# Optimization experiments

Measured on AMD Instinct MI355X. Metric: run time of the kernel, lower is better.

The kernel has to match this reference:

```python
import jax, jax.numpy as jnp
import numpy as np

N_EXPERTS = 8
D_MODEL = 512
HIDDEN = 1408
TOTAL_TOKENS = 32768  # 4096 tokens per expert, equal contiguous segments


def setup_inputs() -> dict:
    key = jax.random.key(0)
    k1, k2, k3 = jax.random.split(key, 3)
    sorted_x = jax.random.normal(k1, (TOTAL_TOKENS, D_MODEL), dtype=jnp.float32)
    # weights init: normal(std=0.02) as in the torch module
    w12 = 0.02 * jax.random.normal(k2, (N_EXPERTS, 2 * HIDDEN, D_MODEL), dtype=jnp.float32)
    w3 = 0.02 * jax.random.normal(k3, (N_EXPERTS, D_MODEL, HIDDEN), dtype=jnp.float32)
    tpe = TOTAL_TOKENS // N_EXPERTS
    expert_starts = jnp.arange(N_EXPERTS, dtype=jnp.int32) * tpe
    expert_ends = expert_starts + tpe
    return {"sorted_x": sorted_x, "w12": w12, "w3": w3,
            "expert_starts": expert_starts, "expert_ends": expert_ends}


def reference(sorted_x, w12, w3, expert_starts, expert_ends):
    """Grouped SwiGLU expert MLP over tokens pre-sorted by expert.

    setup_inputs() produces equal-sized contiguous expert segments, so each
    expert processes tpe = T // E tokens (fixed-size grouped GEMM).
    """
    E, twoH, D = w12.shape
    T = sorted_x.shape[0]
    tpe = T // E  # tokens per expert segment

    # gather each expert's contiguous token block: (E, tpe, D)
    x_e = jax.vmap(lambda s: jax.lax.dynamic_slice(sorted_x, (s, 0), (tpe, D)))(expert_starts)

    # grouped GEMM 1 (fused gate+up): (E, tpe, 2H)
    h12 = jnp.einsum('etd,ehd->eth', x_e, w12).astype(jnp.float32)
    h1, h2 = jnp.split(h12, 2, axis=-1)
    h = jax.nn.silu(h1) * h2  # SwiGLU

    # grouped GEMM 2 (down-proj): (E, tpe, D)
    out = jnp.einsum('eth,edh->etd', h.astype(sorted_x.dtype), w3).astype(jnp.float32)
    # segments are contiguous and in expert order -> concat == reshape
    return out.reshape(T, D)
```

## Files before the change

kernel.cpp:

```cpp
#include <hip/hip_runtime.h>
#include <stdint.h>

#define TPE 4096
#define DM 512
#define HID 1408
#define NE 8

#define N4X   4194304
#define N4W12 2883584

typedef unsigned short u16;
typedef __attribute__((ext_vector_type(8))) __bf16 bf16x8;
typedef __attribute__((ext_vector_type(4))) float f32x4;

__device__ __forceinline__ u16 f2bf(float f) {
  union { float f; uint32_t u; } v; v.f = f;
  uint32_t u = v.u;
  u += 0x7fffu + ((u >> 16) & 1u);
  return (u16)(u >> 16);
}

__global__ void cvt_xw12(const float* __restrict__ x, const float* __restrict__ w12,
                         u16* __restrict__ xb, u16* __restrict__ w12b) {
  int i = blockIdx.x * blockDim.x + threadIdx.x;
  const float* src; u16* dst; int off;
  if (i < N4X) { src = x;   dst = xb;   off = i; }
  else         { src = w12; dst = w12b; off = i - N4X; }
  float4 v = reinterpret_cast<const float4*>(src)[off];
  union { u16 s[4]; uint2 u2; } o;
  o.s[0] = f2bf(v.x); o.s[1] = f2bf(v.y); o.s[2] = f2bf(v.z); o.s[3] = f2bf(v.w);
  reinterpret_cast<uint2*>(dst)[off] = o.u2;
}

template <int ROWS>
__device__ __forceinline__ void stage_tile64(u16* lds, const u16* g, int lda,
                                             int wave, int lane) {
  const int srow = lane >> 3;
  const int gchunk = (lane & 7) ^ srow;
#pragma unroll
  for (int r = 0; r < ROWS / 32; ++r) {
    const int row0 = (wave * (ROWS / 32) + r) * 8;
    const u16* gp = g + (size_t)(row0 + srow) * lda + gchunk * 8;
    u16* lp = lds + row0 * 64;
    __builtin_amdgcn_global_load_lds((const __attribute__((address_space(1))) void*)gp,
                                     (__attribute__((address_space(3))) void*)lp,
                                     16, 0, 0);
  }
}

__device__ __forceinline__ void stage256(u16* lds, const u16* g, int lda,
                                         int wave, int lane) {
  const int srow = lane >> 3;
  const int gchunk = (lane & 7) ^ srow;
#pragma unroll
  for (int r = 0; r < 4; ++r) {
    const int row0 = (r * 8 + wave) * 8;
    const u16* gp = g + (size_t)(row0 + srow) * lda + gchunk * 8;
    u16* lp = lds + row0 * 64;
    __builtin_amdgcn_global_load_lds((const __attribute__((address_space(1))) void*)gp,
                                     (__attribute__((address_space(3))) void*)lp,
                                     16, 0, 0);
  }
}

__device__ __forceinline__ void stageB256(u16* lds, const u16* Bg, const u16* Bu,
                                          int wave, int lane) {
  const int srow = lane >> 3;
  const int gchunk = (lane & 7) ^ srow;
#pragma unroll
  for (int r = 0; r < 4; ++r) {
    const int rowblk = r * 8 + wave;
    const int row0 = rowblk * 8;
    const u16* base = (rowblk < 16) ? (Bg + (size_t)row0 * DM)
                                    : (Bu + (size_t)(row0 - 128) * DM);
    const u16* gp = base + (size_t)srow * DM + gchunk * 8;
    u16* lp = lds + row0 * 64;
    __builtin_amdgcn_global_load_lds((const __attribute__((address_space(1))) void*)gp,
                                     (__attribute__((address_space(3))) void*)lp,
                                     16, 0, 0);
  }
}

__device__ __forceinline__ bf16x8 read_frag(const u16* lds, int row, int kchunk) {
  return *reinterpret_cast<const bf16x8*>(&lds[row * 64 + (((kchunk ^ (row & 7)) << 3))]);
}

__global__ __launch_bounds__(512, 2)
void gemm1_swiglu(const u16* __restrict__ xb, const u16* __restrict__ w12b,
                  u16* __restrict__ hb, const float* __restrict__ w3f,
                  u16* __restrict__ w3b) {
  __shared__ u16 sA[2][256 * 64];
  __shared__ u16 sB[2][256 * 64];
  const int e = blockIdx.x;
  const int y = blockIdx.y;
  const int tid = threadIdx.x;

  if (y >= 176) {
    const int c = e + 8 * (y - 176);
    const float4* src = reinterpret_cast<const float4*>(w3f) + (size_t)c * 4096;
    uint2* dst = reinterpret_cast<uint2*>(w3b) + (size_t)c * 4096;
#pragma unroll
    for (int it = 0; it < 8; ++it) {
      float4 v = src[it * 512 + tid];
      union { u16 s[4]; uint2 u2; } o;
      o.s[0] = f2bf(v.x); o.s[1] = f2bf(v.y); o.s[2] = f2bf(v.z); o.s[3] = f2bf(v.w);
      dst[it * 512 + tid] = o.u2;
    }
    return;
  }

  const int mt = y / 11, nt = y % 11;
  const int wave = tid >> 6, lane = tid & 63;
  const int wm = wave >> 2, wn = wave & 3;
  const int quad = lane >> 4, rr = lane & 15;

  const u16* A  = xb + (size_t)(e * TPE + mt * 256) * DM;
  const u16* Bg = w12b + (size_t)e * (2 * HID) * DM + (size_t)(nt * 128) * DM;
  const u16* Bu = Bg + (size_t)HID * DM;

  f32x4 zero = {0.f, 0.f, 0.f, 0.f};
  f32x4 accg[8][2], accu[8][2];
#pragma unroll
  for (int i = 0; i < 8; ++i)
#pragma unroll
    for (int j = 0; j < 2; ++j) { accg[i][j] = zero; accu[i][j] = zero; }

  stage256(sA[0], A, DM, wave, lane);
  stageB256(sB[0], Bg, Bu, wave, lane);
  __syncthreads();

#pragma unroll 2
  for (int t = 0; t < 8; ++t) {
    const int cur = t & 1, nxt = cur ^ 1;
    const u16* cA = sA[cur];
    const u16* cB = sB[cur];
    bf16x8 af[4][2], bg[2][2], bu[2][2];

    if (t < 7) stage256(sA[nxt], A + (t + 1) * 64, DM, wave, lane);
#pragma unroll
    for (int mi = 0; mi < 4; ++mi)
#pragma unroll
      for (int kk = 0; kk < 2; ++kk)
        af[mi][kk] = read_frag(cA, wm * 128 + mi * 16 + rr, kk * 4 + quad);
#pragma unroll
    for (int ni = 0; ni < 2; ++ni)
#pragma unroll
      for (int kk = 0; kk < 2; ++kk)
        bg[ni][kk] = read_frag(cB, wn * 32 + ni * 16 + rr, kk * 4 + quad);
    __builtin_amdgcn_s_barrier();
    __builtin_amdgcn_s_setprio(1);
#pragma unroll
    for (int mi = 0; mi < 4; ++mi)
#pragma unroll
      for (int ni = 0; ni < 2; ++ni)
#pragma unroll
        for (int kk = 0; kk < 2; ++kk)
          accg[mi][ni] = __builtin_amdgcn_mfma_f32_16x16x32_bf16(af[mi][kk], bg[ni][kk], accg[mi][ni], 0, 0, 0);
    __builtin_amdgcn_s_setprio(0);
    __builtin_amdgcn_s_barrier();

    if (t < 7) stageB256(sB[nxt], Bg + (t + 1) * 64, Bu + (t + 1) * 64, wave, lane);
#pragma unroll
    for (int ni = 0; ni < 2; ++ni)
#pragma unroll
      for (int kk = 0; kk < 2; ++kk)
        bu[ni][kk] = read_frag(cB, 128 + wn * 32 + ni * 16 + rr, kk * 4 + quad);
    __builtin_amdgcn_s_barrier();
    __builtin_amdgcn_s_setprio(1);
#pragma unroll
    for (int mi = 0; mi < 4; ++mi)
#pragma unroll
      for (int ni = 0; ni < 2; ++ni)
#pragma unroll
        for (int kk = 0; kk < 2; ++kk)
          accu[mi][ni] = __builtin_amdgcn_mfma_f32_16x16x32_bf16(af[mi][kk], bu[ni][kk], accu[mi][ni], 0, 0, 0);
    __builtin_amdgcn_s_setprio(0);
    __builtin_amdgcn_s_barrier();

#pragma unroll
    for (int mi = 0; mi < 4; ++mi)
#pragma unroll
      for (int kk = 0; kk < 2; ++kk)
        af[mi][kk] = read_frag(cA, wm * 128 + 64 + mi * 16 + rr, kk * 4 + quad);
    __builtin_amdgcn_s_barrier();
    __builtin_amdgcn_s_setprio(1);
#pragma unroll
    for (int mi = 0; mi < 4; ++mi)
#pragma unroll
      for (int ni = 0; ni < 2; ++ni)
#pragma unroll
        for (int kk = 0; kk < 2; ++kk)
          accg[4 + mi][ni] = __builtin_amdgcn_mfma_f32_16x16x32_bf16(af[mi][kk], bg[ni][kk], accg[4 + mi][ni], 0, 0, 0);
    __builtin_amdgcn_s_setprio(0);
    __builtin_amdgcn_s_barrier();

    __builtin_amdgcn_s_setprio(1);
#pragma unroll
    for (int mi = 0; mi < 4; ++mi)
#pragma unroll
      for (int ni = 0; ni < 2; ++ni)
#pragma unroll
        for (int kk = 0; kk < 2; ++kk)
          accu[4 + mi][ni] = __builtin_amdgcn_mfma_f32_16x16x32_bf16(af[mi][kk], bu[ni][kk], accu[4 + mi][ni], 0, 0, 0);
    __builtin_amdgcn_s_setprio(0);
    __syncthreads();
  }

  const size_t rowbase = (size_t)(e * TPE + mt * 256 + wm * 128);
  const int colbase = nt * 128 + wn * 32;
#pragma unroll
  for (int mi = 0; mi < 8; ++mi)
#pragma unroll
    for (int ni = 0; ni < 2; ++ni)
#pragma unroll
      for (int r2 = 0; r2 < 4; ++r2) {
        float g = accg[mi][ni][r2];
        float u = accu[mi][ni][r2];
        float s = (g / (1.f + __expf(-g))) * u;
        size_t row = rowbase + mi * 16 + quad * 4 + r2;
        int col = colbase + ni * 16 + rr;
        hb[row * HID + col] = f2bf(s);
      }
}

__global__ __launch_bounds__(256, 2)
void gemm2(const u16* __restrict__ hb, const u16* __restrict__ w3b,
           float* __restrict__ out) {
  __shared__ u16 sA[128 * 64];
  __shared__ u16 sB[256 * 64];
  const int e = blockIdx.x;
  const int mt = blockIdx.y >> 1, nt = blockIdx.y & 1;
  const int tid = threadIdx.x, wave = tid >> 6, lane = tid & 63;
  const int wm = wave >> 1, wn = wave & 1;
  const int quad = lane >> 4, rr = lane & 15;

  const u16* A = hb + (size_t)(e * TPE + mt * 128) * HID;
  const u16* B = w3b + (size_t)e * DM * HID + (size_t)(nt * 256) * HID;

  f32x4 zero = {0.f, 0.f, 0.f, 0.f};
  f32x4 acc[4][8];
#pragma unroll
  for (int i = 0; i < 4; ++i)
#pragma unroll
    for (int j = 0; j < 8; ++j) acc[i][j] = zero;

  for (int k0 = 0; k0 < HID; k0 += 64) {
    stage_tile64<128>(sA, A + k0, HID, wave, lane);
    stage_tile64<256>(sB, B + k0, HID, wave, lane);
    __syncthreads();

#pragma unroll
    for (int kk = 0; kk < 2; ++kk) {
      const int kc = kk * 4 + quad;
      bf16x8 af[4], bfr[8];
#pragma unroll
      for (int mi = 0; mi < 4; ++mi)
        af[mi] = read_frag(sA, wm * 64 + mi * 16 + rr, kc);
#pragma unroll
      for (int ni = 0; ni < 8; ++ni)
        bfr[ni] = read_frag(sB, wn * 128 + ni * 16 + rr, kc);
#pragma unroll
      for (int mi = 0; mi < 4; ++mi)
#pragma unroll
        for (int ni = 0; ni < 8; ++ni)
          acc[mi][ni] = __builtin_amdgcn_mfma_f32_16x16x32_bf16(af[mi], bfr[ni], acc[mi][ni], 0, 0, 0);
    }
    __syncthreads();
  }

  const size_t rowbase = (size_t)(e * TPE + mt * 128 + wm * 64);
  const int colbase = nt * 256 + wn * 128;
#pragma unroll
  for (int mi = 0; mi < 4; ++mi)
#pragma unroll
    for (int ni = 0; ni < 8; ++ni)
#pragma unroll
      for (int r2 = 0; r2 < 4; ++r2) {
        size_t row = rowbase + mi * 16 + quad * 4 + r2;
        int col = colbase + ni * 16 + rr;
        out[row * DM + col] = acc[mi][ni][r2];
      }
}

extern "C" void kernel_launch(void* const* d_in, const int* in_sizes, int n_in,
                              void* d_out, int out_size, void* d_ws, size_t ws_size,
                              hipStream_t stream) {
  (void)in_sizes; (void)n_in; (void)out_size; (void)ws_size;
  const float* x   = (const float*)d_in[0];
  const float* w12 = (const float*)d_in[1];
  const float* w3  = (const float*)d_in[2];
  float* out = (float*)d_out;

  char* ws = (char*)d_ws;
  u16* xb   = (u16*)(ws);
  u16* w12b = (u16*)(ws + (size_t)33554432);
  u16* w3b  = (u16*)(ws + (size_t)33554432 + 23068672);
  u16* hb   = (u16*)(ws + (size_t)33554432 + 23068672 + 11534336);

  const int n4 = N4X + N4W12;
  cvt_xw12<<<n4 / 256, 256, 0, stream>>>(x, w12, xb, w12b);

  gemm1_swiglu<<<dim3(8, 176 + 44), 512, 0, stream>>>(xb, w12b, hb, w3, w3b);
  gemm2<<<dim3(8, 64), 256, 0, stream>>>(hb, w3b, out);
}
```

Before: 320.8 us.

## Replace double-buffered K=64 staging with 4-deep K=32 LDS ring in gemm1

The gate/up GEMM kernel moves from a two-stage LDS double buffer with 64-wide K tiles to a four-slot ring of 32-wide K tiles, prefetching three tiles ahead. Fine-grained vmcnt waits replace the full __syncthreads per iteration, so global-to-LDS loads overlap more MFMA work. The per-iteration phase structure drops from four MFMA phases to two. LDS footprint stays the same, but the swizzle width shrinks and barriers per unit of K roughly double, which may add sync overhead. The hand-counted vmcnt values must match the outstanding load counts exactly.

```diff
diff --git a/kernel.cpp b/kernel.cpp
--- a/kernel.cpp
+++ b/kernel.cpp
@@ -48,49 +48,52 @@
   }
 }
 
-__device__ __forceinline__ void stage256(u16* lds, const u16* g, int lda,
+__device__ __forceinline__ bf16x8 read_frag(const u16* lds, int row, int kchunk) {
+  return *reinterpret_cast<const bf16x8*>(&lds[row * 64 + (((kchunk ^ (row & 7)) << 3))]);
+}
+
+__device__ __forceinline__ void stage32A(u16* lds, const u16* g, int lda,
                                          int wave, int lane) {
-  const int srow = lane >> 3;
-  const int gchunk = (lane & 7) ^ srow;
-#pragma unroll
-  for (int r = 0; r < 4; ++r) {
-    const int row0 = (r * 8 + wave) * 8;
+  const int srow = lane >> 2;
+  const int gchunk = (lane & 3) ^ (srow & 3);
+#pragma unroll
+  for (int r = 0; r < 2; ++r) {
+    const int row0 = (r * 8 + wave) * 16;
     const u16* gp = g + (size_t)(row0 + srow) * lda + gchunk * 8;
-    u16* lp = lds + row0 * 64;
+    u16* lp = lds + row0 * 32;
     __builtin_amdgcn_global_load_lds((const __attribute__((address_space(1))) void*)gp,
                                      (__attribute__((address_space(3))) void*)lp,
                                      16, 0, 0);
   }
 }
 
-__device__ __forceinline__ void stageB256(u16* lds, const u16* Bg, const u16* Bu,
-                                          int wave, int lane) {
-  const int srow = lane >> 3;
-  const int gchunk = (lane & 7) ^ srow;
-#pragma unroll
-  for (int r = 0; r < 4; ++r) {
+__device__ __forceinline__ void stage32B(u16* lds, const u16* Bg, const u16* Bu,
+                                         int wave, int lane) {
+  const int srow = lane >> 2;
+  const int gchunk = (lane & 3) ^ (srow & 3);
+#pragma unroll
+  for (int r = 0; r < 2; ++r) {
     const int rowblk = r * 8 + wave;
-    const int row0 = rowblk * 8;
-    const u16* base = (rowblk < 16) ? (Bg + (size_t)row0 * DM)
-                                    : (Bu + (size_t)(row0 - 128) * DM);
+    const int row0 = rowblk * 16;
+    const u16* base = (rowblk < 8) ? (Bg + (size_t)row0 * DM)
+                                   : (Bu + (size_t)(row0 - 128) * DM);
     const u16* gp = base + (size_t)srow * DM + gchunk * 8;
-    u16* lp = lds + row0 * 64;
+    u16* lp = lds + row0 * 32;
     __builtin_amdgcn_global_load_lds((const __attribute__((address_space(1))) void*)gp,
                                      (__attribute__((address_space(3))) void*)lp,
                                      16, 0, 0);
   }
 }
 
-__device__ __forceinline__ bf16x8 read_frag(const u16* lds, int row, int kchunk) {
-  return *reinterpret_cast<const bf16x8*>(&lds[row * 64 + (((kchunk ^ (row & 7)) << 3))]);
+__device__ __forceinline__ bf16x8 read_frag32(const u16* lds, int row, int kc) {
+  return *reinterpret_cast<const bf16x8*>(&lds[row * 32 + ((kc ^ (row & 3)) << 3)]);
 }
 
 __global__ __launch_bounds__(512, 2)
 void gemm1_swiglu(const u16* __restrict__ xb, const u16* __restrict__ w12b,
                   u16* __restrict__ hb, const float* __restrict__ w3f,
                   u16* __restrict__ w3b) {
-  __shared__ u16 sA[2][256 * 64];
-  __shared__ u16 sB[2][256 * 64];
+  __shared__ u16 ring[4][2][256 * 32];
   const int e = blockIdx.x;
   const int y = blockIdx.y;
   const int tid = threadIdx.x;
@@ -125,85 +128,59 @@
 #pragma unroll
     for (int j = 0; j < 2; ++j) { accg[i][j] = zero; accu[i][j] = zero; }
 
-  stage256(sA[0], A, DM, wave, lane);
-  stageB256(sB[0], Bg, Bu, wave, lane);
-  __syncthreads();
-
-#pragma unroll 2
-  for (int t = 0; t < 8; ++t) {
-    const int cur = t & 1, nxt = cur ^ 1;
-    const u16* cA = sA[cur];
-    const u16* cB = sB[cur];
-    bf16x8 af[4][2], bg[2][2], bu[2][2];
-
-    if (t < 7) stage256(sA[nxt], A + (t + 1) * 64, DM, wave, lane);
-#pragma unroll
-    for (int mi = 0; mi < 4; ++mi)
-#pragma unroll
-      for (int kk = 0; kk < 2; ++kk)
-        af[mi][kk] = read_frag(cA, wm * 128 + mi * 16 + rr, kk * 4 + quad);
+#pragma unroll
+  for (int p = 0; p < 3; ++p) {
+    stage32A(ring[p][0], A + p * 32, DM, wave, lane);
+    stage32B(ring[p][1], Bg + p * 32, Bu + p * 32, wave, lane);
+  }
+  asm volatile("s_waitcnt vmcnt(8)" ::: "memory");
+  __builtin_amdgcn_s_barrier();
+
+#pragma unroll 4
+  for (int t = 0; t < 16; ++t) {
+    const u16* RA = ring[t & 3][0];
+    const u16* RB = ring[t & 3][1];
+    u16* WA = ring[(t + 3) & 3][0];
+    u16* WB = ring[(t + 3) & 3][1];
+    bf16x8 af[8], bg[2], bu[2];
+
+    if (t <= 12) stage32A(WA, A + (t + 3) * 32, DM, wave, lane);
+#pragma unroll
+    for (int mi = 0; mi < 8; ++mi)
+      af[mi] = read_frag32(RA, wm * 128 + mi * 16 + rr, quad);
 #pragma unroll
     for (int ni = 0; ni < 2; ++ni)
-#pragma unroll
-      for (int kk = 0; kk < 2; ++kk)
-        bg[ni][kk] = read_frag(cB, wn * 32 + ni * 16 + rr, kk * 4 + quad);
-    __builtin_amdgcn_s_barrier();
+      bg[ni] = read_frag32(RB, wn * 32 + ni * 16 + rr, quad);
+    __builtin_amdgcn_s_barrier();
+    asm volatile("s_waitcnt lgkmcnt(0)" ::: "memory");
+    __builtin_amdgcn_sched_barrier(0);
     __builtin_amdgcn_s_setprio(1);
 #pragma unroll
-    for (int mi = 0; mi < 4; ++mi)
+    for (int mi = 0; mi < 8; ++mi)
 #pragma unroll
       for (int ni = 0; ni < 2; ++ni)
-#pragma unroll
-        for (int kk = 0; kk < 2; ++kk)
-          accg[mi][ni] = __builtin_amdgcn_mfma_f32_16x16x32_bf16(af[mi][kk], bg[ni][kk], accg[mi][ni], 0, 0, 0);
+        accg[mi][ni] = __builtin_amdgcn_mfma_f32_16x16x32_bf16(af[mi], bg[ni], accg[mi][ni], 0, 0, 0);
     __builtin_amdgcn_s_setprio(0);
     __builtin_amdgcn_s_barrier();
 
-    if (t < 7) stageB256(sB[nxt], Bg + (t + 1) * 64, Bu + (t + 1) * 64, wave, lane);
+    if (t <= 12) stage32B(WB, Bg + (t + 3) * 32, Bu + (t + 3) * 32, wave, lane);
 #pragma unroll
     for (int ni = 0; ni < 2; ++ni)
-#pragma unroll
-      for (int kk = 0; kk < 2; ++kk)
-        bu[ni][kk] = read_frag(cB, 128 + wn * 32 + ni * 16 + rr, kk * 4 + quad);
-    __builtin_amdgcn_s_barrier();
+      bu[ni] = read_frag32(RB, 128 + wn * 32 + ni * 16 + rr, quad);
+    __builtin_amdgcn_s_barrier();
+    asm volatile("s_waitcnt lgkmcnt(0)" ::: "memory");
+    __builtin_amdgcn_sched_barrier(0);
     __builtin_amdgcn_s_setprio(1);
 #pragma unroll
-    for (int mi = 0; mi < 4; ++mi)
+    for (int mi = 0; mi < 8; ++mi)
 #pragma unroll
       for (int ni = 0; ni < 2; ++ni)
-#pragma unroll
-        for (int kk = 0; kk < 2; ++kk)
-          accu[mi][ni] = __builtin_amdgcn_mfma_f32_16x16x32_bf16(af[mi][kk], bu[ni][kk], accu[mi][ni], 0, 0, 0);
+        accu[mi][ni] = __builtin_amdgcn_mfma_f32_16x16x32_bf16(af[mi], bu[ni], accu[mi][ni], 0, 0, 0);
     __builtin_amdgcn_s_setprio(0);
-    __builtin_amdgcn_s_barrier();
-
-#pragma unroll
-    for (int mi = 0; mi < 4; ++mi)
-#pragma unroll
-      for (int kk = 0; kk < 2; ++kk)
-        af[mi][kk] = read_frag(cA, wm * 128 + 64 + mi * 16 + rr, kk * 4 + quad);
-    __builtin_amdgcn_s_barrier();
-    __builtin_amdgcn_s_setprio(1);
-#pragma unroll
-    for (int mi = 0; mi < 4; ++mi)
-#pragma unroll
-      for (int ni = 0; ni < 2; ++ni)
-#pragma unroll
-        for (int kk = 0; kk < 2; ++kk)
-          accg[4 + mi][ni] = __builtin_amdgcn_mfma_f32_16x16x32_bf16(af[mi][kk], bg[ni][kk], accg[4 + mi][ni], 0, 0, 0);
-    __builtin_amdgcn_s_setprio(0);
-    __builtin_amdgcn_s_barrier();
-
-    __builtin_amdgcn_s_setprio(1);
-#pragma unroll
-    for (int mi = 0; mi < 4; ++mi)
-#pragma unroll
-      for (int ni = 0; ni < 2; ++ni)
-#pragma unroll
-        for (int kk = 0; kk < 2; ++kk)
-          accu[4 + mi][ni] = __builtin_amdgcn_mfma_f32_16x16x32_bf16(af[mi][kk], bu[ni][kk], accu[4 + mi][ni], 0, 0, 0);
-    __builtin_amdgcn_s_setprio(0);
-    __syncthreads();
+    if (t <= 12)      asm volatile("s_waitcnt vmcnt(8)" ::: "memory");
+    else if (t == 13) asm volatile("s_waitcnt vmcnt(4)" ::: "memory");
+    else if (t == 14) asm volatile("s_waitcnt vmcnt(0)" ::: "memory");
+    __builtin_amdgcn_s_barrier();
   }
 
   const size_t rowbase = (size_t)(e * TPE + mt * 256 + wm * 128);
```

New measurement: 341.3 us. 6.4% more time.
